# Kernel tuning notes

Measured on AMD Instinct MI355X. Metric: run time of the kernel, lower is better.

Reference implementation:

```python
import jax, jax.numpy as jnp
import numpy as np

EMBED_DIM = 1024
NUM_HEADS = 16
HEAD_DIM = EMBED_DIM // NUM_HEADS


def setup_inputs() -> dict:
    key = jax.random.key(0)
    k_x, k_wqkv, k_bqkv, k_wo, k_bo = jax.random.split(key, 5)
    b, n = 2, 2048
    scale_in = 1.0 / np.sqrt(EMBED_DIM)
    return {
        "x": jax.random.normal(k_x, (b, n, EMBED_DIM), dtype=jnp.float32),
        "W_qkv": jax.random.normal(k_wqkv, (EMBED_DIM, 3 * EMBED_DIM), dtype=jnp.float32) * scale_in,
        "b_qkv": jnp.zeros((3 * EMBED_DIM,), dtype=jnp.float32),
        "W_out": jax.random.normal(k_wo, (EMBED_DIM, EMBED_DIM), dtype=jnp.float32) * scale_in,
        "b_out": jnp.zeros((EMBED_DIM,), dtype=jnp.float32),
    }


def _rope_rotate(t, cos, sin):
    # t: [b, h, n, hd]; cos/sin: [1, 1, n, hd//2]
    t1, t2 = jnp.split(t, 2, axis=-1)
    return jnp.concatenate([cos * t1 - sin * t2, sin * t1 + cos * t2], axis=-1)


def reference(x, W_qkv, b_qkv, W_out, b_out):
    b, n, d = x.shape
    h, hd = NUM_HEADS, HEAD_DIM

    qkv = x @ W_qkv + b_qkv                      # [b, n, 3d]
    q, k, v = jnp.split(qkv, 3, axis=-1)
    q, k, v = [t.reshape(b, n, h, hd).transpose(0, 2, 1, 3) for t in (q, k, v)]

    # RoPE tables
    hd2 = hd // 2
    theta = 10000.0 ** (-2.0 * jnp.arange(hd2, dtype=jnp.float32) / hd)
    freqs = jnp.arange(n, dtype=jnp.float32)[:, None] * theta[None, :]  # [n, hd2]
    cos = jnp.cos(freqs)[None, None]
    sin = jnp.sin(freqs)[None, None]
    q = _rope_rotate(q, cos, sin)
    k = _rope_rotate(k, cos, sin)

    scores = jnp.einsum('bhqd,bhkd->bhqk', q, k) / jnp.sqrt(jnp.float32(hd))
    attn = jax.nn.softmax(scores, axis=-1)       # [b, h, n, n]
    out = jnp.einsum('bhqk,bhkd->bhqd', attn, v)
    out = out.transpose(0, 2, 1, 3).reshape(b, n, d)
    return out @ W_out + b_out
```

## Files before the change

kernel.cpp:

```cpp
#include <hip/hip_runtime.h>
#include <hip/hip_bf16.h>
#include <math.h>

#define EMBED 1024
#define NHEAD 16
#define HD 64
#define BATCH 2
#define SEQ 2048
#define MTOT (BATCH * SEQ)
#define QKVN (3 * EMBED)

typedef __attribute__((ext_vector_type(8))) short short8;
typedef __attribute__((ext_vector_type(4))) float f32x4;

typedef __attribute__((address_space(1))) const unsigned int GUI;
typedef __attribute__((address_space(3))) unsigned int LUI;

__device__ __forceinline__ void gload_lds16(const void* src, void* dst) {
  __builtin_amdgcn_global_load_lds((GUI*)src, (LUI*)dst, 16, 0, 0);
}

__device__ __forceinline__ unsigned short f2bf(float f) {
  unsigned u = __builtin_bit_cast(unsigned, f);
  u += 0x7fffu + ((u >> 16) & 1u);
  return (unsigned short)(u >> 16);
}

__device__ __forceinline__ unsigned cvt_pk_bf16(float lo, float hi) {
  unsigned r;
  asm("v_cvt_pk_bf16_f32 %0, %1, %2" : "=v"(r) : "v"(lo), "v"(hi));
  return r;
}

#define QSCALE 0.1803368801111191f


__global__ __launch_bounds__(256) void k_cvt(const float* __restrict__ in,
                                             unsigned short* __restrict__ out, int n4) {
  int i = blockIdx.x * 256 + threadIdx.x;
  if (i >= n4) return;
  float4 v = reinterpret_cast<const float4*>(in)[i];
  ushort4 o;
  o.x = f2bf(v.x); o.y = f2bf(v.y); o.z = f2bf(v.z); o.w = f2bf(v.w);
  reinterpret_cast<ushort4*>(out)[i] = o;
}

__global__ __launch_bounds__(256) void k_transpose_cvt(const float* __restrict__ W,
                                                       unsigned short* __restrict__ WT,
                                                       int K, int Ncols) {
  __shared__ float tile[32][33];
  int n0 = blockIdx.x * 32, k0 = blockIdx.y * 32;
  int tc = threadIdx.x & 31, tr = threadIdx.x >> 5;
  for (int i = 0; i < 4; i++) {
    int r = tr + i * 8;
    tile[r][tc] = W[(size_t)(k0 + r) * Ncols + n0 + tc];
  }
  __syncthreads();
  for (int i = 0; i < 4; i++) {
    int r = tr + i * 8;
    WT[(size_t)(n0 + r) * K + k0 + tc] = f2bf(tile[tc][r]);
  }
}

__global__ __launch_bounds__(256) void k_rope_tables(float* __restrict__ cosT,
                                                     float* __restrict__ sinT) {
  int idx = blockIdx.x * 256 + threadIdx.x;
  if (idx >= SEQ * 32) return;
  int pos = idx >> 5, i = idx & 31;
  float theta = __expf((float)i * -0.28782313662425575f);
  float f = (float)pos * theta;
  cosT[idx] = cosf(f);
  sinT[idx] = sinf(f);
}

__device__ __forceinline__ void gemm_mainloop(const unsigned short* __restrict__ A,
                                              const unsigned short* __restrict__ Bt,
                                              unsigned short* Al, unsigned short* Bl,
                                              size_t m0, size_t n0,
                                              int tid, int l15, int g, int wm, int wn,
                                              f32x4 acc[4][4]) {
  const int w = tid >> 6;
  const int lane = tid & 63;
  const int srow = lane >> 3, slot = lane & 7;
  for (int k0 = 0; k0 < 1024; k0 += 64) {
    __syncthreads();
    for (int it = 0; it < 4; it++) {
      const int r = w * 32 + it * 8 + srow;
      const int sc = (slot ^ (r & 7)) * 8;
      gload_lds16(A + (m0 + r) * 1024 + k0 + sc, &Al[(w * 32 + it * 8) * 64]);
      gload_lds16(Bt + (n0 + r) * 1024 + k0 + sc, &Bl[(w * 32 + it * 8) * 64]);
    }
    __syncthreads();
    for (int kk = 0; kk < 2; kk++) {
      short8 fa[4], fb[4];
      const int xr = ((kk * 4 + g) ^ (l15 & 7)) * 8;
      for (int i = 0; i < 4; i++)
        fa[i] = *reinterpret_cast<const short8*>(&Al[(wm * 64 + i * 16 + l15) * 64 + xr]);
      for (int j = 0; j < 4; j++)
        fb[j] = *reinterpret_cast<const short8*>(&Bl[(wn * 64 + j * 16 + l15) * 64 + xr]);
      for (int i = 0; i < 4; i++)
        for (int j = 0; j < 4; j++)
          acc[i][j] = __builtin_amdgcn_mfma_f32_16x16x32_bf16(fa[i], fb[j], acc[i][j], 0, 0, 0);
    }
  }
}

__global__ __launch_bounds__(256) void k_qkv_gemm(const unsigned short* __restrict__ A,
                                                  const unsigned short* __restrict__ Bt,
                                                  const float* __restrict__ bias,
                                                  const float* __restrict__ cosT,
                                                  const float* __restrict__ sinT,
                                                  unsigned short* __restrict__ Qb,
                                                  unsigned short* __restrict__ Kb,
                                                  unsigned short* __restrict__ Vtg) {
  __shared__ alignas(16) unsigned short Al[128 * 64];
  __shared__ alignas(16) unsigned short Bl[128 * 64];
  const int tid = threadIdx.x;
  const int lane = tid & 63, l15 = lane & 15, g = lane >> 4;
  const int wid = tid >> 6, wm = wid >> 1, wn = wid & 1;
  const size_t m0 = (size_t)blockIdx.y * 128;
  const size_t n0 = (size_t)blockIdx.x * 128;
  f32x4 acc[4][4] = {};
  gemm_mainloop(A, Bt, Al, Bl, m0, n0, tid, l15, g, wm, wn, acc);

  const int cbase = (int)n0 + wn * 64;
  const int sec = cbase >> 10;
  const int head = (cbase & 1023) >> 6;
  float bia[4];
  for (int j = 0; j < 4; j++) bia[j] = bias[cbase + j * 16 + l15];
  const size_t mw = m0 + wm * 64;

  if (sec == 2) {
    const int dsw = ((l15 >> 3) & 1) << 2;
    for (int i = 0; i < 4; i++) {
      size_t mbase = mw + i * 16 + g * 4;
      int bb = (int)(mbase >> 11), pos0 = (int)(mbase & 2047);
      size_t hb = (size_t)(bb * NHEAD + head) * HD;
      for (int j = 0; j < 4; j++) {
        int d = j * 16 + l15;
        uint2 pk;
        pk.x = cvt_pk_bf16(acc[i][j][0] + bia[j], acc[i][j][1] + bia[j]);
        pk.y = cvt_pk_bf16(acc[i][j][2] + bia[j], acc[i][j][3] + bia[j]);
        *reinterpret_cast<uint2*>(Vtg + (hb + d) * SEQ + (pos0 ^ dsw)) = pk;
      }
    }
  } else {
    unsigned short* dst = sec ? Kb : Qb;
    const float qs = sec ? 1.0f : QSCALE;
    for (int i = 0; i < 4; i++)
      for (int r = 0; r < 4; r++) {
        size_t m = mw + i * 16 + g * 4 + r;
        int bb = (int)(m >> 11), pos = (int)(m & 2047);
        size_t base = ((size_t)(bb * NHEAD + head) * SEQ + pos) * HD;
        const float* cr = cosT + pos * 32;
        const float* sr = sinT + pos * 32;
        for (int pl = 0; pl < 2; pl++) {
          int ii = pl * 16 + l15;
          float c = cr[ii], s = sr[ii];
          float lo = acc[i][pl][r] + bia[pl];
          float hi = acc[i][pl + 2][r] + bia[pl + 2];
          dst[base + ii]      = f2bf((c * lo - s * hi) * qs);
          dst[base + 32 + ii] = f2bf((s * lo + c * hi) * qs);
        }
      }
  }
}

__global__ __launch_bounds__(256) void k_out_gemm(const unsigned short* __restrict__ A,
                                                  const unsigned short* __restrict__ Bt,
                                                  const float* __restrict__ bias,
                                                  float* __restrict__ out) {
  __shared__ alignas(16) unsigned short Al[128 * 64];
  __shared__ alignas(16) unsigned short Bl[64 * 64];
  const int tid = threadIdx.x;
  const int lane = tid & 63, l15 = lane & 15, g = lane >> 4;
  const int wid = tid >> 6, wm = wid >> 1, wn = wid & 1;
  const int w = wid;
  const int srow = lane >> 3, slot = lane & 7;
  const size_t m0 = (size_t)blockIdx.y * 128;
  const size_t n0 = (size_t)blockIdx.x * 64;
  f32x4 acc[4][2] = {};

  for (int k0 = 0; k0 < 1024; k0 += 64) {
    __syncthreads();
    for (int it = 0; it < 4; it++) {
      const int r = w * 32 + it * 8 + srow;
      const int sc = (slot ^ (r & 7)) * 8;
      gload_lds16(A + (m0 + r) * 1024 + k0 + sc, &Al[(w * 32 + it * 8) * 64]);
    }
    for (int it = 0; it < 2; it++) {
      const int r = w * 16 + it * 8 + srow;
      const int sc = (slot ^ (r & 7)) * 8;
      gload_lds16(Bt + (n0 + r) * 1024 + k0 + sc, &Bl[(w * 16 + it * 8) * 64]);
    }
    __syncthreads();
    for (int kk = 0; kk < 2; kk++) {
      short8 fa[4], fb[2];
      const int xr = ((kk * 4 + g) ^ (l15 & 7)) * 8;
      for (int i = 0; i < 4; i++)
        fa[i] = *reinterpret_cast<const short8*>(&Al[(wm * 64 + i * 16 + l15) * 64 + xr]);
      for (int j = 0; j < 2; j++)
        fb[j] = *reinterpret_cast<const short8*>(&Bl[(wn * 32 + j * 16 + l15) * 64 + xr]);
      for (int i = 0; i < 4; i++)
        for (int j = 0; j < 2; j++)
          acc[i][j] = __builtin_amdgcn_mfma_f32_16x16x32_bf16(fa[i], fb[j], acc[i][j], 0, 0, 0);
    }
  }

  const int cbase = (int)n0 + wn * 32;
  const size_t mw = m0 + wm * 64;
  for (int i = 0; i < 4; i++)
    for (int r = 0; r < 4; r++) {
      size_t m = mw + i * 16 + g * 4 + r;
      for (int j = 0; j < 2; j++) {
        int col = cbase + j * 16 + l15;
        out[m * EMBED + col] = acc[i][j][r] + bias[col];
      }
    }
}

__global__ __launch_bounds__(256) void k_attn(const unsigned short* __restrict__ Q,
                                              const unsigned short* __restrict__ Kg,
                                              const unsigned short* __restrict__ Vtg,
                                              unsigned short* __restrict__ AO) {
  __shared__ alignas(16) unsigned short Kt[64 * 64];
  __shared__ alignas(16) unsigned short Vt[64 * 64];
  const int tid = threadIdx.x, w = tid >> 6, lane = tid & 63;
  const int l15 = lane & 15, g = lane >> 4;
  const int srow = lane >> 3, slot = lane & 7;

  const int n = blockIdx.x;
  const int xcd = n & 7, rest = n >> 3;
  const int qb = rest & 15, bh = (rest >> 4) * 8 + xcd;

  const unsigned short* Qp = Q + (size_t)bh * SEQ * HD;
  const unsigned short* Kp = Kg + (size_t)bh * SEQ * HD;
  const unsigned short* Vp = Vtg + (size_t)bh * HD * SEQ;
  const int q0 = qb * 128 + w * 32;

  short8 aq[2][2];
#pragma unroll
  for (int u = 0; u < 2; u++)
#pragma unroll
    for (int kk = 0; kk < 2; kk++)
      aq[u][kk] = *reinterpret_cast<const short8*>(
          Qp + (size_t)(q0 + u * 16 + l15) * HD + kk * 32 + g * 8);

  const int sr16 = w * 16 + srow;
  const int sc0 = (slot ^ (sr16 & 7)) * 8;

  f32x4 o[2][4] = {};
  float lrow[2] = {0.f, 0.f};

  for (int t = 0; t < SEQ / 64; t++) {
    const int kb = t * 64;
    __syncthreads();
    gload_lds16(Kp + (size_t)(kb + sr16) * HD + sc0, &Kt[(w * 16) * 64]);
    gload_lds16(Vp + (size_t)sr16 * SEQ + kb + sc0, &Vt[(w * 16) * 64]);
    gload_lds16(Kp + (size_t)(kb + sr16 + 8) * HD + sc0, &Kt[(w * 16 + 8) * 64]);
    gload_lds16(Vp + (size_t)(sr16 + 8) * SEQ + kb + sc0, &Vt[(w * 16 + 8) * 64]);
    __syncthreads();

    f32x4 s[2][4] = {};
#pragma unroll
    for (int kk = 0; kk < 2; kk++) {
      const int xr = ((kk * 4 + g) ^ (l15 & 7)) * 8;
#pragma unroll
      for (int c = 0; c < 4; c++) {
        short8 ak = *reinterpret_cast<const short8*>(&Kt[(c * 16 + l15) * 64 + xr]);
        s[0][c] = __builtin_amdgcn_mfma_f32_16x16x32_bf16(ak, aq[0][kk], s[0][c], 0, 0, 0);
        s[1][c] = __builtin_amdgcn_mfma_f32_16x16x32_bf16(ak, aq[1][kk], s[1][c], 0, 0, 0);
      }
    }

    unsigned wpk[2][8];
#pragma unroll
    for (int u = 0; u < 2; u++) {
      float rs = 0.f;
#pragma unroll
      for (int c = 0; c < 4; c++) {
        float p0 = __builtin_exp2f(s[u][c][0]);
        float p1 = __builtin_exp2f(s[u][c][1]);
        float p2 = __builtin_exp2f(s[u][c][2]);
        float p3 = __builtin_exp2f(s[u][c][3]);
        rs += (p0 + p1) + (p2 + p3);
        wpk[u][2 * c]     = cvt_pk_bf16(p0, p1);
        wpk[u][2 * c + 1] = cvt_pk_bf16(p2, p3);
      }
      lrow[u] += rs;
    }

    const int rx = l15 & 7;
    const int h4 = ((g ^ (l15 >> 3)) & 1) * 4;
#pragma unroll
    for (int kk = 0; kk < 2; kk++) {
      short8 pb0 = __builtin_bit_cast(short8,
          uint4{wpk[0][4 * kk], wpk[0][4 * kk + 1], wpk[0][4 * kk + 2], wpk[0][4 * kk + 3]});
      short8 pb1 = __builtin_bit_cast(short8,
          uint4{wpk[1][4 * kk], wpk[1][4 * kk + 1], wpk[1][4 * kk + 2], wpk[1][4 * kk + 3]});
#pragma unroll
      for (int c2 = 0; c2 < 4; c2++) {
        const unsigned short* vrow = &Vt[(c2 * 16 + l15) * 64];
        uint2 v1 = *reinterpret_cast<const uint2*>(vrow + ((4 * kk + (g >> 1)) ^ rx) * 8 + h4);
        uint2 v2 = *reinterpret_cast<const uint2*>(vrow + ((4 * kk + 2 + (g >> 1)) ^ rx) * 8 + h4);
        short8 av = __builtin_bit_cast(short8, uint4{v1.x, v1.y, v2.x, v2.y});
        o[0][c2] = __builtin_amdgcn_mfma_f32_16x16x32_bf16(av, pb0, o[0][c2], 0, 0, 0);
        o[1][c2] = __builtin_amdgcn_mfma_f32_16x16x32_bf16(av, pb1, o[1][c2], 0, 0, 0);
      }
    }
  }

  const int bb = bh >> 4, h = bh & 15;
#pragma unroll
  for (int u = 0; u < 2; u++) {
    float l = lrow[u];
    l += __shfl_xor(l, 16, 64);
    l += __shfl_xor(l, 32, 64);
    const float inv = 1.f / l;
    const int pos = q0 + u * 16 + l15;
    unsigned short* dst = AO + ((size_t)bb * SEQ + pos) * EMBED + h * HD;
#pragma unroll
    for (int c2 = 0; c2 < 4; c2++) {
      uint2 pk;
      pk.x = cvt_pk_bf16(o[u][c2][0] * inv, o[u][c2][1] * inv);
      pk.y = cvt_pk_bf16(o[u][c2][2] * inv, o[u][c2][3] * inv);
      *reinterpret_cast<uint2*>(dst + c2 * 16 + g * 4) = pk;
    }
  }
}

extern "C" void kernel_launch(void* const* d_in, const int* in_sizes, int n_in,
                              void* d_out, int out_size, void* d_ws, size_t ws_size,
                              hipStream_t stream) {
  const float* x    = (const float*)d_in[0];
  const float* Wqkv = (const float*)d_in[1];
  const float* bqkv = (const float*)d_in[2];
  const float* Wout = (const float*)d_in[3];
  const float* bout = (const float*)d_in[4];
  float* out = (float*)d_out;

  char* ws = (char*)d_ws;
  size_t off = 0;
  auto carve = [&](size_t bytes) {
    char* p = ws + off;
    off += (bytes + 255) & ~(size_t)255;
    return p;
  };
  float* cosT           = (float*)carve((size_t)SEQ * 32 * 4);
  float* sinT           = (float*)carve((size_t)SEQ * 32 * 4);
  unsigned short* Xb    = (unsigned short*)carve((size_t)MTOT * EMBED * 2);
  unsigned short* WqkvT = (unsigned short*)carve((size_t)QKVN * EMBED * 2);
  unsigned short* WoT   = (unsigned short*)carve((size_t)EMBED * EMBED * 2);
  unsigned short* Qb    = (unsigned short*)carve((size_t)MTOT * EMBED * 2);
  unsigned short* Kb    = (unsigned short*)carve((size_t)MTOT * EMBED * 2);
  unsigned short* Vtg   = (unsigned short*)carve((size_t)MTOT * EMBED * 2);
  unsigned short* AO    = (unsigned short*)carve((size_t)MTOT * EMBED * 2);

  k_cvt<<<(MTOT * EMBED / 4 + 255) / 256, 256, 0, stream>>>(x, Xb, MTOT * EMBED / 4);
  k_transpose_cvt<<<dim3(QKVN / 32, EMBED / 32), 256, 0, stream>>>(Wqkv, WqkvT, EMBED, QKVN);
  k_transpose_cvt<<<dim3(EMBED / 32, EMBED / 32), 256, 0, stream>>>(Wout, WoT, EMBED, EMBED);
  k_rope_tables<<<(SEQ * 32) / 256, 256, 0, stream>>>(cosT, sinT);

  k_qkv_gemm<<<dim3(QKVN / 128, MTOT / 128), 256, 0, stream>>>(Xb, WqkvT, bqkv, cosT, sinT, Qb, Kb, Vtg);
  k_attn<<<dim3(512), 256, 0, stream>>>(Qb, Kb, Vtg, AO);
  k_out_gemm<<<dim3(EMBED / 64, MTOT / 128), 256, 0, stream>>>(AO, WoT, bout, out);
}
```

Measured before the change: 150.5 us.

## Split attention over two key halves with a separate merge kernel

Splits the attention key loop into two halves, each handled by its own block, which doubles the attention grid from 512 to 1024 blocks so more of the GPU's compute units stay busy. Each block writes unnormalized fp32 partial outputs and row sums to a new workspace. A new merge kernel adds the two partials, normalizes by the combined row sum, transposes through LDS and writes the bf16 output used by the projection GEMM. In exchange it adds an extra kernel launch and about 16 MB of fp32 partial-output traffic, written with strided, partly coalesced stores.

```diff
diff --git a/kernel.cpp b/kernel.cpp
--- a/kernel.cpp
+++ b/kernel.cpp
@@ -222,7 +222,8 @@
 __global__ __launch_bounds__(256) void k_attn(const unsigned short* __restrict__ Q,
                                               const unsigned short* __restrict__ Kg,
                                               const unsigned short* __restrict__ Vtg,
-                                              unsigned short* __restrict__ AO) {
+                                              float* __restrict__ Opart,
+                                              float* __restrict__ lpart) {
   __shared__ alignas(16) unsigned short Kt[64 * 64];
   __shared__ alignas(16) unsigned short Vt[64 * 64];
   const int tid = threadIdx.x, w = tid >> 6, lane = tid & 63;
@@ -230,8 +231,9 @@
   const int srow = lane >> 3, slot = lane & 7;
 
   const int n = blockIdx.x;
-  const int xcd = n & 7, rest = n >> 3;
-  const int qb = rest & 15, bh = (rest >> 4) * 8 + xcd;
+  const int xcd = n & 7, m = n >> 3;
+  const int qb = m & 15, z = m >> 4;
+  const int sp = z & 1, bh = (z >> 1) * 8 + xcd;
 
   const unsigned short* Qp = Q + (size_t)bh * SEQ * HD;
   const unsigned short* Kp = Kg + (size_t)bh * SEQ * HD;
@@ -252,7 +254,7 @@
   f32x4 o[2][4] = {};
   float lrow[2] = {0.f, 0.f};
 
-  for (int t = 0; t < SEQ / 64; t++) {
+  for (int t = sp * 16; t < sp * 16 + 16; t++) {
     const int kb = t * 64;
     __syncthreads();
     gload_lds16(Kp + (size_t)(kb + sr16) * HD + sc0, &Kt[(w * 16) * 64]);
@@ -310,23 +312,51 @@
     }
   }
 
-  const int bb = bh >> 4, h = bh & 15;
+  const size_t ob = (size_t)(sp * 32 + bh) * HD * SEQ;
 #pragma unroll
   for (int u = 0; u < 2; u++) {
     float l = lrow[u];
     l += __shfl_xor(l, 16, 64);
     l += __shfl_xor(l, 32, 64);
-    const float inv = 1.f / l;
     const int pos = q0 + u * 16 + l15;
-    unsigned short* dst = AO + ((size_t)bb * SEQ + pos) * EMBED + h * HD;
-#pragma unroll
-    for (int c2 = 0; c2 < 4; c2++) {
-      uint2 pk;
-      pk.x = cvt_pk_bf16(o[u][c2][0] * inv, o[u][c2][1] * inv);
-      pk.y = cvt_pk_bf16(o[u][c2][2] * inv, o[u][c2][3] * inv);
-      *reinterpret_cast<uint2*>(dst + c2 * 16 + g * 4) = pk;
-    }
-  }
+    if (g == 0) lpart[(size_t)(sp * 32 + bh) * SEQ + pos] = l;
+#pragma unroll
+    for (int c2 = 0; c2 < 4; c2++)
+#pragma unroll
+      for (int r = 0; r < 4; r++)
+        Opart[ob + (size_t)(c2 * 16 + g * 4 + r) * SEQ + pos] = o[u][c2][r];
+  }
+}
+
+__global__ __launch_bounds__(256) void k_merge(const float* __restrict__ Op,
+                                               const float* __restrict__ lp,
+                                               unsigned short* __restrict__ AO) {
+  __shared__ float T[64][65];
+  __shared__ float Ls[64];
+  const int tid = threadIdx.x;
+  const int bh = blockIdx.x & 31, pt = blockIdx.x >> 5;
+  const int p0 = pt * 64;
+  const size_t b0 = (size_t)bh * HD * SEQ;
+  const size_t b1 = (size_t)(32 + bh) * HD * SEQ;
+  const int pc = tid & 63, dr = tid >> 6;
+#pragma unroll
+  for (int pass = 0; pass < 16; pass++) {
+    const int d = pass * 4 + dr;
+    T[d][pc] = Op[b0 + (size_t)d * SEQ + p0 + pc] + Op[b1 + (size_t)d * SEQ + p0 + pc];
+  }
+  if (tid < 64)
+    Ls[tid] = lp[(size_t)bh * SEQ + p0 + tid] + lp[(size_t)(32 + bh) * SEQ + p0 + tid];
+  __syncthreads();
+  const int pos = tid >> 2, dc = (tid & 3) * 16;
+  const float inv = 1.f / Ls[pos];
+  const int bb = bh >> 4, h = bh & 15;
+  unsigned short* dst = AO + ((size_t)bb * SEQ + p0 + pos) * EMBED + h * HD + dc;
+  unsigned pk[8];
+#pragma unroll
+  for (int i = 0; i < 8; i++)
+    pk[i] = cvt_pk_bf16(T[dc + 2 * i][pos] * inv, T[dc + 2 * i + 1][pos] * inv);
+  *reinterpret_cast<uint4*>(dst) = uint4{pk[0], pk[1], pk[2], pk[3]};
+  *reinterpret_cast<uint4*>(dst + 8) = uint4{pk[4], pk[5], pk[6], pk[7]};
 }
 
 extern "C" void kernel_launch(void* const* d_in, const int* in_sizes, int n_in,
@@ -355,6 +385,8 @@
   unsigned short* Kb    = (unsigned short*)carve((size_t)MTOT * EMBED * 2);
   unsigned short* Vtg   = (unsigned short*)carve((size_t)MTOT * EMBED * 2);
   unsigned short* AO    = (unsigned short*)carve((size_t)MTOT * EMBED * 2);
+  float* Opart          = (float*)carve((size_t)2 * 32 * HD * SEQ * 4);
+  float* lpart          = (float*)carve((size_t)2 * 32 * SEQ * 4);
 
   k_cvt<<<(MTOT * EMBED / 4 + 255) / 256, 256, 0, stream>>>(x, Xb, MTOT * EMBED / 4);
   k_transpose_cvt<<<dim3(QKVN / 32, EMBED / 32), 256, 0, stream>>>(Wqkv, WqkvT, EMBED, QKVN);
@@ -362,6 +394,7 @@
   k_rope_tables<<<(SEQ * 32) / 256, 256, 0, stream>>>(cosT, sinT);
 
   k_qkv_gemm<<<dim3(QKVN / 128, MTOT / 128), 256, 0, stream>>>(Xb, WqkvT, bqkv, cosT, sinT, Qb, Kb, Vtg);
-  k_attn<<<dim3(512), 256, 0, stream>>>(Qb, Kb, Vtg, AO);
+  k_attn<<<dim3(1024), 256, 0, stream>>>(Qb, Kb, Vtg, Opart, lpart);
+  k_merge<<<dim3(1024), 256, 0, stream>>>(Opart, lpart, AO);
   k_out_gemm<<<dim3(EMBED / 64, MTOT / 128), 256, 0, stream>>>(AO, WoT, bout, out);
 }
```

Result: slower. 153.8 us (+2.2%).
